# Optimization experiments

Hardware: AMD Instinct MI355X
Metric: run time of the kernel (lower is better)

Reference implementation:

```python
import jax, jax.numpy as jnp
import numpy as np

DIM = 512
HEADS = 8
DIM_HEAD = 64
HIDDEN = HEADS * DIM_HEAD  # 512
SCALE = DIM_HEAD ** -0.5


def setup_inputs() -> dict:
    key = jax.random.key(0)
    k1, k2, k3 = jax.random.split(key, 3)
    x = jax.random.normal(k1, (4, 2048, DIM), dtype=jnp.float32)
    # torch Linear weight convention: [out_features, in_features], y = x @ W.T
    W_qkv = jax.random.normal(k2, (3 * HIDDEN, DIM), dtype=jnp.float32) * (DIM ** -0.5)
    W_out = jax.random.normal(k3, (DIM, HIDDEN), dtype=jnp.float32) * (HIDDEN ** -0.5)
    return {"x": x, "W_qkv": W_qkv, "W_out": W_out}


def reference(x, W_qkv, W_out):
    b, n, c = x.shape
    qkv = jnp.einsum('bnc,oc->bno', x, W_qkv)  # [b, n, 3*hidden]
    q, k, v = jnp.split(qkv, 3, axis=-1)
    # rearrange 'b n (h c) -> b h c n'
    def to_heads(t):
        return jnp.transpose(t.reshape(b, n, HEADS, DIM_HEAD), (0, 2, 3, 1))
    q, k, v = to_heads(q), to_heads(k), to_heads(v)
    q = q * SCALE
    sim = jnp.einsum('bhcn,bhcj->bhnj', q, k)  # [b, h, n, n]
    attn = jax.nn.softmax(sim, axis=-1)
    out = jnp.einsum('bhnj,bhdj->bhnd', attn, v)  # [b, h, n, d]
    out = jnp.transpose(out, (0, 2, 1, 3)).reshape(b, n, HIDDEN)  # 'b h n d -> b n (h d)'
    return jnp.einsum('bnh,oh->bno', out, W_out)
```

## Files before the change

kernel.cpp:

```cpp
#include <hip/hip_runtime.h>


typedef unsigned short u16;
typedef __attribute__((ext_vector_type(8))) short s16x8;
typedef __attribute__((ext_vector_type(4))) float f32x4;
typedef __attribute__((ext_vector_type(16))) float f32x16;

__device__ __forceinline__ u16 f2bf(float f) {
  unsigned int u = __float_as_uint(f);
  u = (u + 0x7fffu + ((u >> 16) & 1u)) >> 16;
  return (u16)u;
}

__device__ __forceinline__ void gload16(const u16* g, u16* lds_base) {
  __builtin_amdgcn_global_load_lds(
      (const __attribute__((address_space(1))) unsigned int*)g,
      (__attribute__((address_space(3))) unsigned int*)lds_base, 16, 0, 0);
}

__device__ __forceinline__ void permlane32_swap(unsigned& a, unsigned& b) {
  asm volatile("v_permlane32_swap_b32 %0, %1" : "+v"(a), "+v"(b));
}

__global__ __launch_bounds__(256) void cvt_all(
    const float* __restrict__ x, const float* __restrict__ w1,
    const float* __restrict__ w2, u16* __restrict__ xb,
    u16* __restrict__ w1b, u16* __restrict__ w2b) {
  constexpr int N1 = 8192 * 512 / 4, N2 = 1536 * 512 / 4, N3 = 512 * 512 / 4;
  int i = blockIdx.x * 256 + threadIdx.x;
  if (i >= N1 + N2 + N3) return;
  const float* src;
  u16* dst;
  int j;
  if (i < N1) { src = x; dst = xb; j = i; }
  else if (i < N1 + N2) { src = w1; dst = w1b; j = i - N1; }
  else { src = w2; dst = w2b; j = i - N1 - N2; }
  float4 f = ((const float4*)src)[j];
  uint2 o;
  o.x = (unsigned)f2bf(f.x) | ((unsigned)f2bf(f.y) << 16);
  o.y = (unsigned)f2bf(f.z) | ((unsigned)f2bf(f.w) << 16);
  ((uint2*)dst)[j] = o;
}

template <int BN, int MODE>
__global__ __launch_bounds__(256) void gemm128(
    const u16* __restrict__ A, const u16* __restrict__ B,
    float* __restrict__ Cf,
    u16* __restrict__ Qp, u16* __restrict__ Kp, u16* __restrict__ Vp) {
  constexpr int K = 512;
  constexpr int JN = BN / 32;
  __shared__ u16 smem[128 * 64 + BN * 64];
  u16* As = smem;
  u16* Bs = smem + 128 * 64;
  const int bm0 = blockIdx.x * 128, bn0 = blockIdx.y * BN;
  const int t = threadIdx.x, wave = t >> 6, lane = t & 63;
  const int quad = lane >> 4, l16 = lane & 15;
  const int wm = (wave & 1) * 64, wn = (wave >> 1) * (BN / 2);
  const int lr = lane >> 3, lc = lane & 7;
  const int swz = lc ^ lr;

  f32x4 acc[4][JN] = {};

  for (int k0 = 0; k0 < K; k0 += 64) {
    __syncthreads();
#pragma unroll
    for (int a = 0; a < 4; a++) {
      int r = wave * 32 + a * 8 + lr;
      gload16(A + (size_t)(bm0 + r) * K + k0 + swz * 8,
              &As[(wave * 32 + a * 8) * 64]);
    }
#pragma unroll
    for (int b = 0; b < BN / 32; b++) {
      int r = wave * (BN / 4) + b * 8 + lr;
      gload16(B + (size_t)(bn0 + r) * K + k0 + swz * 8,
              &Bs[(wave * (BN / 4) + b * 8) * 64]);
    }
    __syncthreads();
#pragma unroll
    for (int ks = 0; ks < 2; ks++) {
      s16x8 af[4], bf[JN];
#pragma unroll
      for (int i = 0; i < 4; i++) {
        int m = wm + i * 16 + l16;
        af[i] = *(const s16x8*)(&As[m * 64 + (((ks * 4 + quad) ^ (m & 7)) * 8)]);
      }
#pragma unroll
      for (int j = 0; j < JN; j++) {
        int n = wn + j * 16 + l16;
        bf[j] = *(const s16x8*)(&Bs[n * 64 + (((ks * 4 + quad) ^ (n & 7)) * 8)]);
      }
#pragma unroll
      for (int i = 0; i < 4; i++)
#pragma unroll
        for (int j = 0; j < JN; j++)
          acc[i][j] = __builtin_amdgcn_mfma_f32_16x16x32_bf16(af[i], bf[j], acc[i][j], 0, 0, 0);
    }
  }

  if constexpr (MODE == 1) {
#pragma unroll
    for (int i = 0; i < 4; i++)
#pragma unroll
      for (int j = 0; j < JN; j++)
#pragma unroll
        for (int r = 0; r < 4; r++) {
          int m = bm0 + wm + i * 16 + quad * 4 + r;
          int n = bn0 + wn + j * 16 + l16;
          Cf[(size_t)m * 512 + n] = acc[i][j][r];
        }
  } else {
    const int part = bn0 >> 9;
    if (part < 2) {
#pragma unroll
      for (int i = 0; i < 4; i++)
#pragma unroll
        for (int j = 0; j < JN; j++)
#pragma unroll
          for (int r = 0; r < 4; r++) {
            int m = bm0 + wm + i * 16 + quad * 4 + r;
            int n = bn0 + wn + j * 16 + l16;
            int oin = n & 511;
            int head = oin >> 6, dh = oin & 63;
            int bb = m >> 11, tok = m & 2047;
            size_t idx = ((size_t)(bb * 8 + head) * 2048 + tok) * 64 + dh;
            if (part == 0)
              Qp[idx] = f2bf(acc[i][j][r] * 0.18033688011112042f);
            else
              Kp[idx] = f2bf(acc[i][j][r]);
          }
    } else {
      __syncthreads();
#pragma unroll
      for (int i = 0; i < 4; i++)
#pragma unroll
        for (int j = 0; j < JN; j++)
#pragma unroll
          for (int r = 0; r < 4; r++) {
            int row = wm + i * 16 + quad * 4 + r;
            int cn = wn + j * 16 + l16;
            smem[row * 128 + (cn ^ (row & 7))] = f2bf(acc[i][j][r]);
          }
      __syncthreads();
      const int bb = bm0 >> 11;
      const int tokbase = bm0 & 2047;
      const int headbase = (bn0 & 511) >> 6;
#pragma unroll
      for (int it = 0; it < 8; it++) {
        int cn = it * 16 + (t >> 4);
        int dh = cn & 63, head = headbase + (cn >> 6);
        int tok0 = (t & 15) * 8;
        s16x8 pk;
#pragma unroll
        for (int k = 0; k < 8; k++) {
          int row = tok0 + k;
          pk[k] = (short)smem[row * 128 + (cn ^ (row & 7))];
        }
        *(s16x8*)(&Vp[((size_t)(bb * 8 + head) * 64 + dh) * 2048 + tokbase + tok0]) = pk;
      }
    }
  }
}

__global__ __launch_bounds__(256) void attn_kernel(
    const u16* __restrict__ Qg, const u16* __restrict__ Kg,
    const u16* __restrict__ Vtg, u16* __restrict__ Og) {
  __shared__ __attribute__((aligned(16))) u16 smem[3 * 64 * 72];
  u16* Qs = smem;
  u16* Ks = smem + 64 * 72;
  u16* Vt = smem + 2 * 64 * 72;
  float* Obuf = (float*)smem;
  float* Lbuf = (float*)((char*)smem + 64 * 68 * 4);

  const int id = blockIdx.x;
  const int xcd = id & 7, slot = id >> 3;
  const int bh = xcd * 4 + (slot & 3);
  const int q0 = (slot >> 2) * 64;

  const u16* Qh = Qg + (size_t)bh * 2048 * 64;
  const u16* Kh = Kg + (size_t)bh * 2048 * 64;
  const u16* Vh = Vtg + (size_t)bh * 64 * 2048;
  const int t = threadIdx.x, lane = t & 63, wave = t >> 6;
  const int wq = wave & 1, wk = wave >> 1;
  const int l32 = lane & 31, half = lane >> 5;
  const int srow = t >> 2, scolb = (t & 3) * 8;
  const int q = wq * 32 + l32;

#pragma unroll
  for (int p = 0; p < 2; p++) {
    int col = scolb + p * 32;
    *(s16x8*)(&Qs[srow * 72 + col]) = *(const s16x8*)(Qh + (size_t)(q0 + srow) * 64 + col);
  }
  __syncthreads();
  s16x8 bQ[4];
#pragma unroll
  for (int ks = 0; ks < 4; ks++)
    bQ[ks] = *(const s16x8*)(&Qs[q * 72 + ks * 16 + half * 8]);

  f32x16 o[2] = {};
  float l_acc = 0.f;

  for (int j0 = 0; j0 < 2048; j0 += 64) {
    __syncthreads();
#pragma unroll
    for (int p = 0; p < 2; p++) {
      int col = scolb + p * 32;
      *(s16x8*)(&Ks[srow * 72 + col]) = *(const s16x8*)(Kh + (size_t)(j0 + srow) * 64 + col);
      *(s16x8*)(&Vt[srow * 72 + col]) = *(const s16x8*)(Vh + (size_t)srow * 2048 + j0 + col);
    }
    __syncthreads();

    f32x16 s = {};
#pragma unroll
    for (int ks = 0; ks < 4; ks++) {
      s16x8 aK = *(const s16x8*)(&Ks[(wk * 32 + l32) * 72 + ks * 16 + half * 8]);
      s = __builtin_amdgcn_mfma_f32_32x32x16_bf16(aK, bQ[ks], s, 0, 0, 0);
    }

    unsigned pu[16];
#pragma unroll
    for (int r = 0; r < 16; r++) {
      float p = __builtin_amdgcn_exp2f(s[r]);
      unsigned u = __float_as_uint(p);
      l_acc += __uint_as_float(u & 0xffff0000u);
      pu[r] = u;
    }
    unsigned g[8];
#pragma unroll
    for (int v = 0; v < 8; v++)
      g[v] = __builtin_amdgcn_perm(pu[2 * v + 1], pu[2 * v], 0x07060302u);
    permlane32_swap(g[0], g[2]);
    permlane32_swap(g[1], g[3]);
    permlane32_swap(g[4], g[6]);
    permlane32_swap(g[5], g[7]);
    s16x8 bP[2];
    ((unsigned*)&bP[0])[0] = g[0]; ((unsigned*)&bP[0])[1] = g[1];
    ((unsigned*)&bP[0])[2] = g[2]; ((unsigned*)&bP[0])[3] = g[3];
    ((unsigned*)&bP[1])[0] = g[4]; ((unsigned*)&bP[1])[1] = g[5];
    ((unsigned*)&bP[1])[2] = g[6]; ((unsigned*)&bP[1])[3] = g[7];

#pragma unroll
    for (int dt = 0; dt < 2; dt++)
#pragma unroll
      for (int s2 = 0; s2 < 2; s2++) {
        s16x8 aV = *(const s16x8*)(&Vt[(dt * 32 + l32) * 72 + wk * 32 + s2 * 16 + half * 8]);
        o[dt] = __builtin_amdgcn_mfma_f32_32x32x16_bf16(aV, bP[s2], o[dt], 0, 0, 0);
      }
  }

  __syncthreads();
  Lbuf[(wk * 2 + half) * 64 + q] = l_acc;
  if (wk == 1) {
#pragma unroll
    for (int dt = 0; dt < 2; dt++)
#pragma unroll
      for (int gi = 0; gi < 4; gi++) {
        int d0 = 8 * gi + 4 * half + 32 * dt;
        float4 v = { o[dt][4 * gi + 0], o[dt][4 * gi + 1],
                     o[dt][4 * gi + 2], o[dt][4 * gi + 3] };
        *(float4*)(&Obuf[q * 68 + d0]) = v;
      }
  }
  __syncthreads();
  if (wk == 0) {
    float l = Lbuf[0 * 64 + q] + Lbuf[1 * 64 + q] + Lbuf[2 * 64 + q] + Lbuf[3 * 64 + q];
    float sc = __builtin_amdgcn_rcpf(l);
#pragma unroll
    for (int dt = 0; dt < 2; dt++)
#pragma unroll
      for (int gi = 0; gi < 4; gi++) {
        int d0 = 8 * gi + 4 * half + 32 * dt;
        float4 v = *(float4*)(&Obuf[q * 68 + d0]);
        v.x = (v.x + o[dt][4 * gi + 0]) * sc;
        v.y = (v.y + o[dt][4 * gi + 1]) * sc;
        v.z = (v.z + o[dt][4 * gi + 2]) * sc;
        v.w = (v.w + o[dt][4 * gi + 3]) * sc;
        *(float4*)(&Obuf[q * 68 + d0]) = v;
      }
  }
  __syncthreads();

  {
    const int bb = bh >> 3, h = bh & 7;
    int qq = t >> 2, d0 = (t & 3) * 16;
    float f[16];
#pragma unroll
    for (int c = 0; c < 4; c++) {
      float4 v = *(float4*)(&Obuf[qq * 68 + d0 + 4 * c]);
      f[4 * c + 0] = v.x; f[4 * c + 1] = v.y; f[4 * c + 2] = v.z; f[4 * c + 3] = v.w;
    }
    unsigned pk[8];
#pragma unroll
    for (int c = 0; c < 8; c++)
      pk[c] = (unsigned)f2bf(f[2 * c]) | ((unsigned)f2bf(f[2 * c + 1]) << 16);
    size_t base = ((size_t)bb * 2048 + q0 + qq) * 512 + h * 64 + d0;
    uint4 s0 = { pk[0], pk[1], pk[2], pk[3] };
    uint4 s1 = { pk[4], pk[5], pk[6], pk[7] };
    *(uint4*)(&Og[base]) = s0;
    *(uint4*)(&Og[base + 8]) = s1;
  }
}

extern "C" void kernel_launch(void* const* d_in, const int* in_sizes, int n_in,
                              void* d_out, int out_size, void* d_ws, size_t ws_size,
                              hipStream_t stream) {
  const float* x    = (const float*)d_in[0];
  const float* Wqkv = (const float*)d_in[1];
  const float* Wout = (const float*)d_in[2];
  float* y = (float*)d_out;

  char* ws = (char*)d_ws;
  size_t off = 0;
  auto alloc = [&](size_t bytes) {
    void* p = ws + off;
    off += (bytes + 255) & ~(size_t)255;
    return p;
  };
  u16* xb    = (u16*)alloc((size_t)8192 * 512 * 2);
  u16* wqkvb = (u16*)alloc((size_t)1536 * 512 * 2);
  u16* woutb = (u16*)alloc((size_t)512 * 512 * 2);
  u16* Qw    = (u16*)alloc((size_t)32 * 2048 * 64 * 2);
  u16* Kw    = (u16*)alloc((size_t)32 * 2048 * 64 * 2);
  u16* Vw    = (u16*)alloc((size_t)32 * 2048 * 64 * 2);
  u16* Ow    = (u16*)alloc((size_t)8192 * 512 * 2);
  if (off > ws_size) return;

  cvt_all<<<5120, 256, 0, stream>>>(x, Wqkv, Wout, xb, wqkvb, woutb);

  gemm128<128, 0><<<dim3(64, 12), 256, 0, stream>>>(xb, wqkvb, nullptr, Qw, Kw, Vw);
  attn_kernel<<<1024, 256, 0, stream>>>(Qw, Kw, Vw, Ow);
  gemm128<64, 1><<<dim3(64, 8), 256, 0, stream>>>(Ow, woutb, y, nullptr, nullptr, nullptr);
}
```

Before: 168.6 us.

## Stage Q/K epilogue through LDS and use direct-to-LDS swizzled loads in attention

```diff
diff --git a/kernel.cpp b/kernel.cpp
--- a/kernel.cpp
+++ b/kernel.cpp
@@ -52,7 +52,9 @@
   __shared__ u16 smem[128 * 64 + BN * 64];
   u16* As = smem;
   u16* Bs = smem + 128 * 64;
-  const int bm0 = blockIdx.x * 128, bn0 = blockIdx.y * BN;
+  const int id = blockIdx.x;
+  const int bm0 = (id & 63) * 128;
+  const int bn0 = (id >> 6) * BN;
   const int t = threadIdx.x, wave = t >> 6, lane = t & 63;
   const int quad = lane >> 4, l16 = lane & 15;
   const int wm = (wave & 1) * 64, wn = (wave >> 1) * (BN / 2);
@@ -111,23 +113,33 @@
   } else {
     const int part = bn0 >> 9;
     if (part < 2) {
+      const float qs = (part == 0) ? 0.18033688011112042f : 1.0f;
+      __syncthreads();
 #pragma unroll
       for (int i = 0; i < 4; i++)
 #pragma unroll
         for (int j = 0; j < JN; j++)
 #pragma unroll
           for (int r = 0; r < 4; r++) {
-            int m = bm0 + wm + i * 16 + quad * 4 + r;
-            int n = bn0 + wn + j * 16 + l16;
-            int oin = n & 511;
-            int head = oin >> 6, dh = oin & 63;
-            int bb = m >> 11, tok = m & 2047;
-            size_t idx = ((size_t)(bb * 8 + head) * 2048 + tok) * 64 + dh;
-            if (part == 0)
-              Qp[idx] = f2bf(acc[i][j][r] * 0.18033688011112042f);
-            else
-              Kp[idx] = f2bf(acc[i][j][r]);
+            int row = wm + i * 16 + quad * 4 + r;
+            int cn = wn + j * 16 + l16;
+            smem[row * 128 + (((cn >> 3) ^ (row & 7)) << 3) + (cn & 7)] =
+                f2bf(acc[i][j][r] * qs);
           }
+      __syncthreads();
+      u16* dst = (part == 0) ? Qp : Kp;
+      const int bb = bm0 >> 11;
+      const int tokbase = bm0 & 2047;
+      const int headbase = (bn0 & 511) >> 6;
+#pragma unroll
+      for (int it = 0; it < 8; it++) {
+        int row = it * 16 + (t >> 4);
+        int n0 = (t & 15) * 8;
+        s16x8 pk = *(const s16x8*)(&smem[row * 128 + ((((n0 >> 3) ^ (row & 7))) << 3)]);
+        int head = headbase + (n0 >> 6), dh = n0 & 63;
+        int tok = tokbase + row;
+        *(s16x8*)(&dst[((size_t)(bb * 8 + head) * 2048 + tok) * 64 + dh]) = pk;
+      }
     } else {
       __syncthreads();
 #pragma unroll
@@ -164,10 +176,10 @@
 __global__ __launch_bounds__(256) void attn_kernel(
     const u16* __restrict__ Qg, const u16* __restrict__ Kg,
     const u16* __restrict__ Vtg, u16* __restrict__ Og) {
-  __shared__ __attribute__((aligned(16))) u16 smem[3 * 64 * 72];
+  __shared__ __attribute__((aligned(16))) u16 smem[64 * 72 + 2 * 8 * 520];
   u16* Qs = smem;
   u16* Ks = smem + 64 * 72;
-  u16* Vt = smem + 2 * 64 * 72;
+  u16* Vt = Ks + 8 * 520;
   float* Obuf = (float*)smem;
   float* Lbuf = (float*)((char*)smem + 64 * 68 * 4);
 
@@ -183,6 +195,7 @@
   const int wq = wave & 1, wk = wave >> 1;
   const int l32 = lane & 31, half = lane >> 5;
   const int srow = t >> 2, scolb = (t & 3) * 8;
+  const int lr = lane >> 3, lc = lane & 7, swz = lc ^ lr;
   const int q = wq * 32 + l32;
 
 #pragma unroll
@@ -201,19 +214,24 @@
 
   for (int j0 = 0; j0 < 2048; j0 += 64) {
     __syncthreads();
-#pragma unroll
-    for (int p = 0; p < 2; p++) {
-      int col = scolb + p * 32;
-      *(s16x8*)(&Ks[srow * 72 + col]) = *(const s16x8*)(Kh + (size_t)(j0 + srow) * 64 + col);
-      *(s16x8*)(&Vt[srow * 72 + col]) = *(const s16x8*)(Vh + (size_t)srow * 2048 + j0 + col);
+    {
+      int g0 = wave * 2, g1 = wave * 2 + 1;
+      gload16(Kh + (size_t)(j0 + g0 * 8 + lr) * 64 + swz * 8, &Ks[g0 * 520]);
+      gload16(Kh + (size_t)(j0 + g1 * 8 + lr) * 64 + swz * 8, &Ks[g1 * 520]);
+      gload16(Vh + (size_t)(g0 * 8 + lr) * 2048 + j0 + swz * 8, &Vt[g0 * 520]);
+      gload16(Vh + (size_t)(g1 * 8 + lr) * 2048 + j0 + swz * 8, &Vt[g1 * 520]);
     }
     __syncthreads();
 
     f32x16 s = {};
-#pragma unroll
-    for (int ks = 0; ks < 4; ks++) {
-      s16x8 aK = *(const s16x8*)(&Ks[(wk * 32 + l32) * 72 + ks * 16 + half * 8]);
-      s = __builtin_amdgcn_mfma_f32_32x32x16_bf16(aK, bQ[ks], s, 0, 0, 0);
+    {
+      const int rK = wk * 32 + l32;
+      const int base = (rK >> 3) * 520 + (rK & 7) * 64;
+#pragma unroll
+      for (int ks = 0; ks < 4; ks++) {
+        s16x8 aK = *(const s16x8*)(&Ks[base + (((ks * 2 + half) ^ (rK & 7)) * 8)]);
+        s = __builtin_amdgcn_mfma_f32_32x32x16_bf16(aK, bQ[ks], s, 0, 0, 0);
+      }
     }
 
     unsigned pu[16];
@@ -239,12 +257,15 @@
     ((unsigned*)&bP[1])[2] = g[6]; ((unsigned*)&bP[1])[3] = g[7];
 
 #pragma unroll
-    for (int dt = 0; dt < 2; dt++)
+    for (int dt = 0; dt < 2; dt++) {
+      const int rV = dt * 32 + l32;
+      const int base = (rV >> 3) * 520 + (rV & 7) * 64;
 #pragma unroll
       for (int s2 = 0; s2 < 2; s2++) {
-        s16x8 aV = *(const s16x8*)(&Vt[(dt * 32 + l32) * 72 + wk * 32 + s2 * 16 + half * 8]);
+        s16x8 aV = *(const s16x8*)(&Vt[base + (((wk * 4 + s2 * 2 + half) ^ (rV & 7)) * 8)]);
         o[dt] = __builtin_amdgcn_mfma_f32_32x32x16_bf16(aV, bP[s2], o[dt], 0, 0, 0);
       }
+    }
   }
 
   __syncthreads();
@@ -326,7 +347,7 @@
 
   cvt_all<<<5120, 256, 0, stream>>>(x, Wqkv, Wout, xb, wqkvb, woutb);
 
-  gemm128<128, 0><<<dim3(64, 12), 256, 0, stream>>>(xb, wqkvb, nullptr, Qw, Kw, Vw);
+  gemm128<128, 0><<<768, 256, 0, stream>>>(xb, wqkvb, nullptr, Qw, Kw, Vw);
   attn_kernel<<<1024, 256, 0, stream>>>(Qw, Kw, Vw, Ow);
-  gemm128<64, 1><<<dim3(64, 8), 256, 0, stream>>>(Ow, woutb, y, nullptr, nullptr, nullptr);
-}
+  gemm128<64, 1><<<512, 256, 0, stream>>>(Ow, woutb, y, nullptr, nullptr, nullptr);
+}
```

New measurement: 161.2 us. 4.4% less time.
